# Kernel tuning notes

Hardware: AMD Instinct MI355X
Metric: run time of the kernel (lower is better)

## Reference

```python
import jax, jax.numpy as jnp
import numpy as np

N_DETS = 50000
K_NEIGH = 32
E = N_DETS * K_NEIGH  # 1,600,000 pairs


def _linear_params(key, fan_in, fan_out):
    kw, kb = jax.random.split(key)
    scale = 1.0 / np.sqrt(fan_in)
    W = jax.random.uniform(kw, (fan_in, fan_out), jnp.float32, -scale, scale)
    b = jax.random.uniform(kb, (fan_out,), jnp.float32, -scale, scale)
    return W, b


def setup_inputs() -> dict:
    key = jax.random.key(0)
    ks = jax.random.split(key, 10)
    detFeatures = jax.random.normal(ks[0], (N_DETS, 128), jnp.float32)
    # each detection is the center of exactly K_NEIGH pairs (sorted segment ids)
    cIdxs = jnp.repeat(jnp.arange(N_DETS, dtype=jnp.int32), K_NEIGH)
    nIdxs = jax.random.randint(ks[1], (E,), 0, N_DETS, jnp.int32)
    pairFeatures = jax.random.normal(ks[2], (E, 32), jnp.float32)
    W1, b1 = _linear_params(ks[3], 128, 32)   # fc1: 128 -> 32
    Wp0, bp0 = _linear_params(ks[4], 96, 64)  # pwfeat fc 0: 3*32 -> 64
    Wp1, bp1 = _linear_params(ks[5], 64, 64)  # pwfeat fc 1
    Wq0, bq0 = _linear_params(ks[6], 64, 64)  # postmax fc 0
    Wq1, bq1 = _linear_params(ks[7], 64, 64)  # postmax fc 1
    Wo, bo = _linear_params(ks[8], 64, 128)   # output FC: 64 -> 128
    return {"detFeatures": detFeatures, "cIdxs": cIdxs, "nIdxs": nIdxs,
            "pairFeatures": pairFeatures,
            "W1": W1, "b1": b1, "Wp0": Wp0, "bp0": bp0, "Wp1": Wp1, "bp1": bp1,
            "Wq0": Wq0, "bq0": bq0, "Wq1": Wq1, "bq1": bq1, "Wo": Wo, "bo": bo}


def reference(detFeatures, cIdxs, nIdxs, pairFeatures,
              W1, b1, Wp0, bp0, Wp1, bp1, Wq0, bq0, Wq1, bq1, Wo, bo):
    relu = jax.nn.relu
    # fc1 shortcut reduce: [N,128] -> [N,32]
    f1 = relu(detFeatures @ W1 + b1)
    # gather center/neighbor feats and concat with pair feats: [E, 96]
    comb = jnp.concatenate([pairFeatures, f1[cIdxs], f1[nIdxs]], axis=1)
    h = relu(comb @ Wp0 + bp0)   # [E, 64]
    h = relu(h @ Wp1 + bp1)      # [E, 64]
    # per-detection segment max (replaces the Python loop in the original)
    pooled = jax.ops.segment_max(h, cIdxs, num_segments=detFeatures.shape[0])
    p = relu(pooled @ Wq0 + bq0)
    p = relu(p @ Wq1 + bq1)
    refined = p @ Wo + bo        # [N, 128]
    return relu(detFeatures + refined)
```

## Files before the change

### kernel.cpp

```cpp
#include <hip/hip_runtime.h>
#include <hip/hip_bf16.h>

typedef __attribute__((ext_vector_type(4))) float f32x4;
typedef __attribute__((ext_vector_type(8))) short bf16x8;
typedef __attribute__((ext_vector_type(2))) unsigned int uint2v;

#define N_DETS  50000
#define E_PAIRS 1600000
#define NB64    (E_PAIRS / 64)

__device__ __forceinline__ unsigned short f2bf(float f){
  union { float f; unsigned int u; } v; v.f = f;
  return (unsigned short)((v.u + 0x7FFFu + ((v.u >> 16) & 1u)) >> 16);
}

__device__ __forceinline__ bf16x8 pack8(f32x4 a, f32x4 b){
  union { unsigned int u[4]; bf16x8 v; } t;
  t.u[0] = (unsigned int)f2bf(a[0]) | ((unsigned int)f2bf(a[1]) << 16);
  t.u[1] = (unsigned int)f2bf(a[2]) | ((unsigned int)f2bf(a[3]) << 16);
  t.u[2] = (unsigned int)f2bf(b[0]) | ((unsigned int)f2bf(b[1]) << 16);
  t.u[3] = (unsigned int)f2bf(b[2]) | ((unsigned int)f2bf(b[3]) << 16);
  return t.v;
}

__global__ __launch_bounds__(256) void kA(const float* __restrict__ det,
                                          const float* __restrict__ W1,
                                          const float* __restrict__ b1,
                                          unsigned short* __restrict__ f1){
  __shared__ float w[128*32];
  __shared__ float dt[16][132];
  const int t  = threadIdx.x;
  const int r0 = blockIdx.x * 16;
  {
    const f32x4* ws = reinterpret_cast<const f32x4*>(W1);
    #pragma unroll
    for (int i = 0; i < 4; ++i)
      reinterpret_cast<f32x4*>(w)[t + 256*i] = ws[t + 256*i];
    #pragma unroll
    for (int i = 0; i < 2; ++i){
      int idx = t + 256*i;
      int row = idx >> 5, c4 = (idx & 31) * 4;
      *reinterpret_cast<f32x4*>(&dt[row][c4]) =
        *reinterpret_cast<const f32x4*>(&det[(size_t)(r0+row)*128 + c4]);
    }
  }
  __syncthreads();
  const int r = t >> 4, c2 = (t & 15) * 2;
  float s0 = b1[c2], s1 = b1[c2 + 1];
  #pragma unroll 8
  for (int k = 0; k < 128; ++k){
    float d = dt[r][k];
    s0 = fmaf(d, w[k*32 + c2],     s0);
    s1 = fmaf(d, w[k*32 + c2 + 1], s1);
  }
  s0 = fmaxf(s0, 0.f); s1 = fmaxf(s1, 0.f);
  unsigned int pk = (unsigned int)f2bf(s0) | ((unsigned int)f2bf(s1) << 16);
  *reinterpret_cast<unsigned int*>(&f1[(size_t)(r0+r)*32 + c2]) = pk;
}

__global__ __launch_bounds__(256) void kPack(const float* __restrict__ Wp0,
                                             const float* __restrict__ Wp1,
                                             unsigned short* __restrict__ wf){
  int i = blockIdx.x * 256 + threadIdx.x;
  if (i >= 20*512) return;
  int f = i >> 9;
  int l = (i >> 3) & 63;
  int j = i & 7;
  int lc = l & 15, q = l >> 4;
  float v;
  if (f < 12){
    int kt = f >> 2, ot = f & 3;
    v = Wp0[(kt*32 + q*8 + j)*64 + ot*16 + lc];
  } else {
    int g = f - 12;
    int kt = g >> 2, n2 = g & 3;
    v = Wp1[(kt*32 + q*8 + j)*64 + n2*16 + lc];
  }
  wf[i] = f2bf(v);
}

__global__ __launch_bounds__(256) void kB(const float* __restrict__ pf,
                                          const int*   __restrict__ nIdxs,
                                          const unsigned short* __restrict__ f1,
                                          const unsigned short* __restrict__ wf,
                                          const float* __restrict__ bp0,
                                          const float* __restrict__ bp1,
                                          float* __restrict__ pooled){
  __shared__ __align__(16) unsigned short h1buf[4][4096];
  const int tid  = threadIdx.x;
  const int wid  = tid >> 6;
  const int lane = tid & 63;
  const int lc   = lane & 15;
  const int q    = lane >> 4;
  char* hb = reinterpret_cast<char*>(&h1buf[wid][0]);

  const bf16x8* wfv = reinterpret_cast<const bf16x8*>(wf);
  bf16x8 A0[3][4], B1w[2][4];
  #pragma unroll
  for (int kt = 0; kt < 3; ++kt)
    #pragma unroll
    for (int ot = 0; ot < 4; ++ot)
      A0[kt][ot] = wfv[(kt*4 + ot)*64 + lane];
  #pragma unroll
  for (int kt = 0; kt < 2; ++kt)
    #pragma unroll
    for (int n2 = 0; n2 < 4; ++n2)
      B1w[kt][n2] = wfv[(12 + kt*4 + n2)*64 + lane];

  f32x4 bb0[4];
  #pragma unroll
  for (int ot = 0; ot < 4; ++ot)
    bb0[ot] = *reinterpret_cast<const f32x4*>(&bp0[ot*16 + q*4]);
  float bb1[4];
  #pragma unroll
  for (int n2 = 0; n2 < 4; ++n2) bb1[n2] = bp1[n2*16 + lc];

  const int nwaves = gridDim.x * 4;
  for (int b = blockIdx.x*4 + wid; b < NB64; b += nwaves){
    const int e0 = b * 64;

    f32x4 acc[4][4];
    #pragma unroll
    for (int ot = 0; ot < 4; ++ot)
      #pragma unroll
      for (int et = 0; et < 4; ++et) acc[ot][et] = bb0[ot];

    #pragma unroll
    for (int et = 0; et < 4; ++et){
      const int eg = e0 + et*16 + lc;
      f32x4 p0 = *reinterpret_cast<const f32x4*>(&pf[(size_t)eg*32 + q*8]);
      f32x4 p1 = *reinterpret_cast<const f32x4*>(&pf[(size_t)eg*32 + q*8 + 4]);
      bf16x8 bfr0 = pack8(p0, p1);
      const int c = eg >> 5;
      bf16x8 bfr1 = *reinterpret_cast<const bf16x8*>(&f1[(size_t)c*32 + q*8]);
      const int n = nIdxs[eg];
      bf16x8 bfr2 = *reinterpret_cast<const bf16x8*>(&f1[(size_t)n*32 + q*8]);
      #pragma unroll
      for (int ot = 0; ot < 4; ++ot){
        acc[ot][et] = __builtin_amdgcn_mfma_f32_16x16x32_bf16(A0[0][ot], bfr0, acc[ot][et], 0,0,0);
        acc[ot][et] = __builtin_amdgcn_mfma_f32_16x16x32_bf16(A0[1][ot], bfr1, acc[ot][et], 0,0,0);
        acc[ot][et] = __builtin_amdgcn_mfma_f32_16x16x32_bf16(A0[2][ot], bfr2, acc[ot][et], 0,0,0);
      }
    }

    #pragma unroll
    for (int ot = 0; ot < 4; ++ot){
      #pragma unroll
      for (int et = 0; et < 4; ++et){
        f32x4 v = acc[ot][et];
        unsigned int lo = (unsigned int)f2bf(fmaxf(v[0],0.f)) | ((unsigned int)f2bf(fmaxf(v[1],0.f)) << 16);
        unsigned int hi = (unsigned int)f2bf(fmaxf(v[2],0.f)) | ((unsigned int)f2bf(fmaxf(v[3],0.f)) << 16);
        uint2v wv; wv[0] = lo; wv[1] = hi;
        int edge = et*16 + lc;
        int byte = (edge*128 + ot*32 + q*8) ^ ((edge & 7) << 4);
        *reinterpret_cast<uint2v*>(hb + byte) = wv;
      }
    }

    f32x4 acc2[4][4];
    #pragma unroll
    for (int m = 0; m < 4; ++m)
      #pragma unroll
      for (int n2 = 0; n2 < 4; ++n2){
        f32x4 ini = {bb1[n2], bb1[n2], bb1[n2], bb1[n2]};
        acc2[m][n2] = ini;
      }
    #pragma unroll
    for (int m = 0; m < 4; ++m){
      int edge = m*16 + lc;
      int swz  = (edge & 7) << 4;
      bf16x8 a0 = *reinterpret_cast<const bf16x8*>(hb + ((edge*128 + q*16)      ^ swz));
      bf16x8 a1 = *reinterpret_cast<const bf16x8*>(hb + ((edge*128 + 64 + q*16) ^ swz));
      #pragma unroll
      for (int n2 = 0; n2 < 4; ++n2){
        acc2[m][n2] = __builtin_amdgcn_mfma_f32_16x16x32_bf16(a0, B1w[0][n2], acc2[m][n2], 0,0,0);
        acc2[m][n2] = __builtin_amdgcn_mfma_f32_16x16x32_bf16(a1, B1w[1][n2], acc2[m][n2], 0,0,0);
      }
    }

    const int cbase = e0 >> 5;
    #pragma unroll
    for (int cen = 0; cen < 2; ++cen){
      float s0n, s1n, s2n, s3n;
      #pragma unroll
      for (int n2 = 0; n2 < 4; ++n2){
        float m0 = fmaxf(fmaxf(acc2[cen*2][n2][0], acc2[cen*2+1][n2][0]),
                         fmaxf(acc2[cen*2][n2][1], acc2[cen*2+1][n2][1]));
        float m1 = fmaxf(fmaxf(acc2[cen*2][n2][2], acc2[cen*2+1][n2][2]),
                         fmaxf(acc2[cen*2][n2][3], acc2[cen*2+1][n2][3]));
        float mm = fmaxf(m0, m1);
        mm = fmaxf(mm, __shfl_xor(mm, 16));
        mm = fmaxf(mm, __shfl_xor(mm, 32));
        if (n2 == 0) s0n = mm; else if (n2 == 1) s1n = mm; else if (n2 == 2) s2n = mm; else s3n = mm;
      }
      float v01 = (q & 1) ? s1n : s0n;
      float v23 = (q & 1) ? s3n : s2n;
      float v   = (q & 2) ? v23 : v01;
      v = fmaxf(v, 0.f);
      pooled[(size_t)(cbase + cen)*64 + lane] = v;
    }
  }
}

__global__ __launch_bounds__(256) void kC(const float* __restrict__ det,
                                          const float* __restrict__ pooled,
                                          const float* __restrict__ Wq0, const float* __restrict__ bq0,
                                          const float* __restrict__ Wq1, const float* __restrict__ bq1,
                                          const float* __restrict__ Wo,  const float* __restrict__ bo,
                                          float* __restrict__ out){
  __shared__ float w0[4096];
  __shared__ float w1[4096];
  __shared__ float wo2[8192];
  __shared__ float bb[256];
  __shared__ float pt[16*68];
  __shared__ float p1t[16*68];
  const int t  = threadIdx.x;
  const int r0 = blockIdx.x * 16;
  {
    const f32x4* s0 = reinterpret_cast<const f32x4*>(Wq0);
    const f32x4* s1 = reinterpret_cast<const f32x4*>(Wq1);
    const f32x4* s2 = reinterpret_cast<const f32x4*>(Wo);
    #pragma unroll
    for (int i = 0; i < 4; ++i) reinterpret_cast<f32x4*>(w0)[t + 256*i] = s0[t + 256*i];
    #pragma unroll
    for (int i = 0; i < 4; ++i) reinterpret_cast<f32x4*>(w1)[t + 256*i] = s1[t + 256*i];
    #pragma unroll
    for (int i = 0; i < 8; ++i) reinterpret_cast<f32x4*>(wo2)[t + 256*i] = s2[t + 256*i];
    if (t < 64)       bb[t] = bq0[t];
    else if (t < 128) bb[t] = bq1[t - 64];
    else              bb[t] = bo[t - 128];
    int row = t >> 4, c4l = (t & 15) * 4;
    *reinterpret_cast<f32x4*>(&pt[row*68 + c4l]) =
      *reinterpret_cast<const f32x4*>(&pooled[(size_t)(r0+row)*64 + c4l]);
  }
  __syncthreads();
  const int r  = t >> 4;
  const int c4 = (t & 15) * 4;

  f32x4 a = *reinterpret_cast<const f32x4*>(&bb[c4]);
  #pragma unroll 8
  for (int k = 0; k < 64; ++k){
    float pd = pt[r*68 + k];
    f32x4 wv = *reinterpret_cast<const f32x4*>(&w0[k*64 + c4]);
    a[0] = fmaf(pd, wv[0], a[0]); a[1] = fmaf(pd, wv[1], a[1]);
    a[2] = fmaf(pd, wv[2], a[2]); a[3] = fmaf(pd, wv[3], a[3]);
  }
  a[0]=fmaxf(a[0],0.f); a[1]=fmaxf(a[1],0.f); a[2]=fmaxf(a[2],0.f); a[3]=fmaxf(a[3],0.f);
  *reinterpret_cast<f32x4*>(&p1t[r*68 + c4]) = a;
  __syncthreads();

  f32x4 a2 = *reinterpret_cast<const f32x4*>(&bb[64 + c4]);
  #pragma unroll 8
  for (int k = 0; k < 64; ++k){
    float pd = p1t[r*68 + k];
    f32x4 wv = *reinterpret_cast<const f32x4*>(&w1[k*64 + c4]);
    a2[0] = fmaf(pd, wv[0], a2[0]); a2[1] = fmaf(pd, wv[1], a2[1]);
    a2[2] = fmaf(pd, wv[2], a2[2]); a2[3] = fmaf(pd, wv[3], a2[3]);
  }
  a2[0]=fmaxf(a2[0],0.f); a2[1]=fmaxf(a2[1],0.f); a2[2]=fmaxf(a2[2],0.f); a2[3]=fmaxf(a2[3],0.f);
  *reinterpret_cast<f32x4*>(&pt[r*68 + c4]) = a2;
  __syncthreads();

  f32x4 o0 = *reinterpret_cast<const f32x4*>(&bb[128 + c4]);
  f32x4 o1 = *reinterpret_cast<const f32x4*>(&bb[128 + 64 + c4]);
  #pragma unroll 8
  for (int k = 0; k < 64; ++k){
    float pd = pt[r*68 + k];
    f32x4 wa = *reinterpret_cast<const f32x4*>(&wo2[k*128 + c4]);
    f32x4 wb = *reinterpret_cast<const f32x4*>(&wo2[k*128 + 64 + c4]);
    o0[0] = fmaf(pd, wa[0], o0[0]); o0[1] = fmaf(pd, wa[1], o0[1]);
    o0[2] = fmaf(pd, wa[2], o0[2]); o0[3] = fmaf(pd, wa[3], o0[3]);
    o1[0] = fmaf(pd, wb[0], o1[0]); o1[1] = fmaf(pd, wb[1], o1[1]);
    o1[2] = fmaf(pd, wb[2], o1[2]); o1[3] = fmaf(pd, wb[3], o1[3]);
  }
  const float* dr = &det[(size_t)(r0 + r) * 128];
  f32x4 d0 = *reinterpret_cast<const f32x4*>(&dr[c4]);
  f32x4 d1 = *reinterpret_cast<const f32x4*>(&dr[64 + c4]);
  f32x4 res0, res1;
  res0[0]=fmaxf(d0[0]+o0[0],0.f); res0[1]=fmaxf(d0[1]+o0[1],0.f);
  res0[2]=fmaxf(d0[2]+o0[2],0.f); res0[3]=fmaxf(d0[3]+o0[3],0.f);
  res1[0]=fmaxf(d1[0]+o1[0],0.f); res1[1]=fmaxf(d1[1]+o1[1],0.f);
  res1[2]=fmaxf(d1[2]+o1[2],0.f); res1[3]=fmaxf(d1[3]+o1[3],0.f);
  float* orow = &out[(size_t)(r0 + r) * 128];
  *reinterpret_cast<f32x4*>(&orow[c4])      = res0;
  *reinterpret_cast<f32x4*>(&orow[64 + c4]) = res1;
}

extern "C" void kernel_launch(void* const* d_in, const int* in_sizes, int n_in,
                              void* d_out, int out_size, void* d_ws, size_t ws_size,
                              hipStream_t stream){
  const float* det   = (const float*)d_in[0];
  const int*   nIdx  = (const int*)  d_in[2];
  const float* pfeat = (const float*)d_in[3];
  const float* W1    = (const float*)d_in[4];
  const float* b1    = (const float*)d_in[5];
  const float* Wp0   = (const float*)d_in[6];
  const float* bp0   = (const float*)d_in[7];
  const float* Wp1   = (const float*)d_in[8];
  const float* bp1   = (const float*)d_in[9];
  const float* Wq0   = (const float*)d_in[10];
  const float* bq0   = (const float*)d_in[11];
  const float* Wq1   = (const float*)d_in[12];
  const float* bq1   = (const float*)d_in[13];
  const float* Wo    = (const float*)d_in[14];
  const float* bo    = (const float*)d_in[15];
  float* out = (float*)d_out;

  unsigned short* f1 = (unsigned short*)d_ws;
  unsigned short* wf = (unsigned short*)((char*)d_ws + 3200000);
  float* pooled      = (float*)((char*)d_ws + 3225600);

  kA   <<<N_DETS/16, 256, 0, stream>>>(det, W1, b1, f1);
  kPack<<<40,        256, 0, stream>>>(Wp0, Wp1, wf);
  kB   <<<1024,      256, 0, stream>>>(pfeat, nIdx, f1, wf, bp0, bp1, pooled);
  kC   <<<N_DETS/16, 256, 0, stream>>>(det, pooled, Wq0, bq0, Wq1, bq1, Wo, bo, out);
}
```

Baseline: 450.2 us.

## Fold weight packing into kA, restructure kB for occupancy, read kC weights directly

Moves the weight-packing kernel into the first blocks of kA, which removes one launch. kB is restructured: neighbor index loads are hoisted ahead of the first layer, accumulators are processed per edge tile, and the second layer is computed per center pair. The bp1 bias is now added after the max, which is valid because max commutes with adding a per-column constant. These changes cut register pressure so launch_bounds can request 3 blocks per SM, and the grid grows to 3125 blocks. kC no longer stages its weights in LDS and reads them through the cache, trading LDS traffic and occupancy limits for global and L1 reads.

```diff
diff --git a/kernel.cpp b/kernel.cpp
--- a/kernel.cpp
+++ b/kernel.cpp
@@ -26,7 +26,28 @@
 __global__ __launch_bounds__(256) void kA(const float* __restrict__ det,
                                           const float* __restrict__ W1,
                                           const float* __restrict__ b1,
-                                          unsigned short* __restrict__ f1){
+                                          const float* __restrict__ Wp0,
+                                          const float* __restrict__ Wp1,
+                                          unsigned short* __restrict__ f1,
+                                          unsigned short* __restrict__ wf){
+  if (blockIdx.x < 40){
+    int i = blockIdx.x * 256 + threadIdx.x;
+    int f = i >> 9;
+    int l = (i >> 3) & 63;
+    int j = i & 7;
+    int plc = l & 15, pq = l >> 4;
+    float v;
+    if (f < 12){
+      int kt = f >> 2, ot = f & 3;
+      v = Wp0[(kt*32 + pq*8 + j)*64 + ot*16 + plc];
+    } else {
+      int g = f - 12;
+      int kt = g >> 2, n2 = g & 3;
+      v = Wp1[(kt*32 + pq*8 + j)*64 + n2*16 + plc];
+    }
+    wf[i] = f2bf(v);
+  }
+
   __shared__ float w[128*32];
   __shared__ float dt[16][132];
   const int t  = threadIdx.x;
@@ -58,34 +79,13 @@
   *reinterpret_cast<unsigned int*>(&f1[(size_t)(r0+r)*32 + c2]) = pk;
 }
 
-__global__ __launch_bounds__(256) void kPack(const float* __restrict__ Wp0,
-                                             const float* __restrict__ Wp1,
-                                             unsigned short* __restrict__ wf){
-  int i = blockIdx.x * 256 + threadIdx.x;
-  if (i >= 20*512) return;
-  int f = i >> 9;
-  int l = (i >> 3) & 63;
-  int j = i & 7;
-  int lc = l & 15, q = l >> 4;
-  float v;
-  if (f < 12){
-    int kt = f >> 2, ot = f & 3;
-    v = Wp0[(kt*32 + q*8 + j)*64 + ot*16 + lc];
-  } else {
-    int g = f - 12;
-    int kt = g >> 2, n2 = g & 3;
-    v = Wp1[(kt*32 + q*8 + j)*64 + n2*16 + lc];
-  }
-  wf[i] = f2bf(v);
-}
-
-__global__ __launch_bounds__(256) void kB(const float* __restrict__ pf,
-                                          const int*   __restrict__ nIdxs,
-                                          const unsigned short* __restrict__ f1,
-                                          const unsigned short* __restrict__ wf,
-                                          const float* __restrict__ bp0,
-                                          const float* __restrict__ bp1,
-                                          float* __restrict__ pooled){
+__global__ __launch_bounds__(256, 3) void kB(const float* __restrict__ pf,
+                                             const int*   __restrict__ nIdxs,
+                                             const unsigned short* __restrict__ f1,
+                                             const unsigned short* __restrict__ wf,
+                                             const float* __restrict__ bp0,
+                                             const float* __restrict__ bp1,
+                                             float* __restrict__ pooled){
   __shared__ __align__(16) unsigned short h1buf[4][4096];
   const int tid  = threadIdx.x;
   const int wid  = tid >> 6;
@@ -111,83 +111,81 @@
   #pragma unroll
   for (int ot = 0; ot < 4; ++ot)
     bb0[ot] = *reinterpret_cast<const f32x4*>(&bp0[ot*16 + q*4]);
-  float bb1[4];
-  #pragma unroll
-  for (int n2 = 0; n2 < 4; ++n2) bb1[n2] = bp1[n2*16 + lc];
+  const float bb1s = bp1[lane];
 
   const int nwaves = gridDim.x * 4;
   for (int b = blockIdx.x*4 + wid; b < NB64; b += nwaves){
     const int e0 = b * 64;
 
-    f32x4 acc[4][4];
-    #pragma unroll
-    for (int ot = 0; ot < 4; ++ot)
-      #pragma unroll
-      for (int et = 0; et < 4; ++et) acc[ot][et] = bb0[ot];
+    int nid[4];
+    #pragma unroll
+    for (int et = 0; et < 4; ++et) nid[et] = nIdxs[e0 + et*16 + lc];
+    bf16x8 f1n[4];
+    #pragma unroll
+    for (int et = 0; et < 4; ++et)
+      f1n[et] = *reinterpret_cast<const bf16x8*>(&f1[(size_t)nid[et]*32 + q*8]);
 
     #pragma unroll
     for (int et = 0; et < 4; ++et){
       const int eg = e0 + et*16 + lc;
       f32x4 p0 = *reinterpret_cast<const f32x4*>(&pf[(size_t)eg*32 + q*8]);
       f32x4 p1 = *reinterpret_cast<const f32x4*>(&pf[(size_t)eg*32 + q*8 + 4]);
+      const int c = (e0 >> 5) + (et >> 1);
+      bf16x8 f1c = *reinterpret_cast<const bf16x8*>(&f1[(size_t)c*32 + q*8]);
       bf16x8 bfr0 = pack8(p0, p1);
-      const int c = eg >> 5;
-      bf16x8 bfr1 = *reinterpret_cast<const bf16x8*>(&f1[(size_t)c*32 + q*8]);
-      const int n = nIdxs[eg];
-      bf16x8 bfr2 = *reinterpret_cast<const bf16x8*>(&f1[(size_t)n*32 + q*8]);
+
+      f32x4 acc[4];
+      #pragma unroll
+      for (int ot = 0; ot < 4; ++ot) acc[ot] = bb0[ot];
       #pragma unroll
       for (int ot = 0; ot < 4; ++ot){
-        acc[ot][et] = __builtin_amdgcn_mfma_f32_16x16x32_bf16(A0[0][ot], bfr0, acc[ot][et], 0,0,0);
-        acc[ot][et] = __builtin_amdgcn_mfma_f32_16x16x32_bf16(A0[1][ot], bfr1, acc[ot][et], 0,0,0);
-        acc[ot][et] = __builtin_amdgcn_mfma_f32_16x16x32_bf16(A0[2][ot], bfr2, acc[ot][et], 0,0,0);
-      }
-    }
-
-    #pragma unroll
-    for (int ot = 0; ot < 4; ++ot){
-      #pragma unroll
-      for (int et = 0; et < 4; ++et){
-        f32x4 v = acc[ot][et];
+        acc[ot] = __builtin_amdgcn_mfma_f32_16x16x32_bf16(A0[0][ot], bfr0,    acc[ot], 0,0,0);
+        acc[ot] = __builtin_amdgcn_mfma_f32_16x16x32_bf16(A0[1][ot], f1c,     acc[ot], 0,0,0);
+        acc[ot] = __builtin_amdgcn_mfma_f32_16x16x32_bf16(A0[2][ot], f1n[et], acc[ot], 0,0,0);
+      }
+
+      const int edge = et*16 + lc;
+      const int swz  = (edge & 7) << 4;
+      #pragma unroll
+      for (int ot = 0; ot < 4; ++ot){
+        f32x4 v = acc[ot];
         unsigned int lo = (unsigned int)f2bf(fmaxf(v[0],0.f)) | ((unsigned int)f2bf(fmaxf(v[1],0.f)) << 16);
         unsigned int hi = (unsigned int)f2bf(fmaxf(v[2],0.f)) | ((unsigned int)f2bf(fmaxf(v[3],0.f)) << 16);
         uint2v wv; wv[0] = lo; wv[1] = hi;
-        int edge = et*16 + lc;
-        int byte = (edge*128 + ot*32 + q*8) ^ ((edge & 7) << 4);
-        *reinterpret_cast<uint2v*>(hb + byte) = wv;
-      }
-    }
-
-    f32x4 acc2[4][4];
-    #pragma unroll
-    for (int m = 0; m < 4; ++m)
+        *reinterpret_cast<uint2v*>(hb + ((edge*128 + ot*32 + q*8) ^ swz)) = wv;
+      }
+    }
+
+    const int cbase = e0 >> 5;
+    #pragma unroll
+    for (int cen = 0; cen < 2; ++cen){
+      const int eA = (2*cen)*16 + lc;
+      const int eB = (2*cen + 1)*16 + lc;
+      const int sw = (lc & 7) << 4;
+      bf16x8 a0A = *reinterpret_cast<const bf16x8*>(hb + ((eA*128      + q*16) ^ sw));
+      bf16x8 a1A = *reinterpret_cast<const bf16x8*>(hb + ((eA*128 + 64 + q*16) ^ sw));
+      bf16x8 a0B = *reinterpret_cast<const bf16x8*>(hb + ((eB*128      + q*16) ^ sw));
+      bf16x8 a1B = *reinterpret_cast<const bf16x8*>(hb + ((eB*128 + 64 + q*16) ^ sw));
+
+      f32x4 accA[4], accB[4];
       #pragma unroll
       for (int n2 = 0; n2 < 4; ++n2){
-        f32x4 ini = {bb1[n2], bb1[n2], bb1[n2], bb1[n2]};
-        acc2[m][n2] = ini;
-      }
-    #pragma unroll
-    for (int m = 0; m < 4; ++m){
-      int edge = m*16 + lc;
-      int swz  = (edge & 7) << 4;
-      bf16x8 a0 = *reinterpret_cast<const bf16x8*>(hb + ((edge*128 + q*16)      ^ swz));
-      bf16x8 a1 = *reinterpret_cast<const bf16x8*>(hb + ((edge*128 + 64 + q*16) ^ swz));
+        f32x4 z = {0.f, 0.f, 0.f, 0.f};
+        accA[n2] = z; accB[n2] = z;
+      }
       #pragma unroll
       for (int n2 = 0; n2 < 4; ++n2){
-        acc2[m][n2] = __builtin_amdgcn_mfma_f32_16x16x32_bf16(a0, B1w[0][n2], acc2[m][n2], 0,0,0);
-        acc2[m][n2] = __builtin_amdgcn_mfma_f32_16x16x32_bf16(a1, B1w[1][n2], acc2[m][n2], 0,0,0);
-      }
-    }
-
-    const int cbase = e0 >> 5;
-    #pragma unroll
-    for (int cen = 0; cen < 2; ++cen){
+        accA[n2] = __builtin_amdgcn_mfma_f32_16x16x32_bf16(a0A, B1w[0][n2], accA[n2], 0,0,0);
+        accA[n2] = __builtin_amdgcn_mfma_f32_16x16x32_bf16(a1A, B1w[1][n2], accA[n2], 0,0,0);
+        accB[n2] = __builtin_amdgcn_mfma_f32_16x16x32_bf16(a0B, B1w[0][n2], accB[n2], 0,0,0);
+        accB[n2] = __builtin_amdgcn_mfma_f32_16x16x32_bf16(a1B, B1w[1][n2], accB[n2], 0,0,0);
+      }
+
       float s0n, s1n, s2n, s3n;
       #pragma unroll
       for (int n2 = 0; n2 < 4; ++n2){
-        float m0 = fmaxf(fmaxf(acc2[cen*2][n2][0], acc2[cen*2+1][n2][0]),
-                         fmaxf(acc2[cen*2][n2][1], acc2[cen*2+1][n2][1]));
-        float m1 = fmaxf(fmaxf(acc2[cen*2][n2][2], acc2[cen*2+1][n2][2]),
-                         fmaxf(acc2[cen*2][n2][3], acc2[cen*2+1][n2][3]));
+        float m0 = fmaxf(fmaxf(accA[n2][0], accB[n2][0]), fmaxf(accA[n2][1], accB[n2][1]));
+        float m1 = fmaxf(fmaxf(accA[n2][2], accB[n2][2]), fmaxf(accA[n2][3], accB[n2][3]));
         float mm = fmaxf(m0, m1);
         mm = fmaxf(mm, __shfl_xor(mm, 16));
         mm = fmaxf(mm, __shfl_xor(mm, 32));
@@ -196,7 +194,7 @@
       float v01 = (q & 1) ? s1n : s0n;
       float v23 = (q & 1) ? s3n : s2n;
       float v   = (q & 2) ? v23 : v01;
-      v = fmaxf(v, 0.f);
+      v = fmaxf(v + bb1s, 0.f);
       pooled[(size_t)(cbase + cen)*64 + lane] = v;
     }
   }
@@ -208,27 +206,11 @@
                                           const float* __restrict__ Wq1, const float* __restrict__ bq1,
                                           const float* __restrict__ Wo,  const float* __restrict__ bo,
                                           float* __restrict__ out){
-  __shared__ float w0[4096];
-  __shared__ float w1[4096];
-  __shared__ float wo2[8192];
-  __shared__ float bb[256];
   __shared__ float pt[16*68];
   __shared__ float p1t[16*68];
   const int t  = threadIdx.x;
   const int r0 = blockIdx.x * 16;
   {
-    const f32x4* s0 = reinterpret_cast<const f32x4*>(Wq0);
-    const f32x4* s1 = reinterpret_cast<const f32x4*>(Wq1);
-    const f32x4* s2 = reinterpret_cast<const f32x4*>(Wo);
-    #pragma unroll
-    for (int i = 0; i < 4; ++i) reinterpret_cast<f32x4*>(w0)[t + 256*i] = s0[t + 256*i];
-    #pragma unroll
-    for (int i = 0; i < 4; ++i) reinterpret_cast<f32x4*>(w1)[t + 256*i] = s1[t + 256*i];
-    #pragma unroll
-    for (int i = 0; i < 8; ++i) reinterpret_cast<f32x4*>(wo2)[t + 256*i] = s2[t + 256*i];
-    if (t < 64)       bb[t] = bq0[t];
-    else if (t < 128) bb[t] = bq1[t - 64];
-    else              bb[t] = bo[t - 128];
     int row = t >> 4, c4l = (t & 15) * 4;
     *reinterpret_cast<f32x4*>(&pt[row*68 + c4l]) =
       *reinterpret_cast<const f32x4*>(&pooled[(size_t)(r0+row)*64 + c4l]);
@@ -237,11 +219,11 @@
   const int r  = t >> 4;
   const int c4 = (t & 15) * 4;
 
-  f32x4 a = *reinterpret_cast<const f32x4*>(&bb[c4]);
+  f32x4 a = *reinterpret_cast<const f32x4*>(&bq0[c4]);
   #pragma unroll 8
   for (int k = 0; k < 64; ++k){
     float pd = pt[r*68 + k];
-    f32x4 wv = *reinterpret_cast<const f32x4*>(&w0[k*64 + c4]);
+    f32x4 wv = *reinterpret_cast<const f32x4*>(&Wq0[k*64 + c4]);
     a[0] = fmaf(pd, wv[0], a[0]); a[1] = fmaf(pd, wv[1], a[1]);
     a[2] = fmaf(pd, wv[2], a[2]); a[3] = fmaf(pd, wv[3], a[3]);
   }
@@ -249,11 +231,11 @@
   *reinterpret_cast<f32x4*>(&p1t[r*68 + c4]) = a;
   __syncthreads();
 
-  f32x4 a2 = *reinterpret_cast<const f32x4*>(&bb[64 + c4]);
+  f32x4 a2 = *reinterpret_cast<const f32x4*>(&bq1[c4]);
   #pragma unroll 8
   for (int k = 0; k < 64; ++k){
     float pd = p1t[r*68 + k];
-    f32x4 wv = *reinterpret_cast<const f32x4*>(&w1[k*64 + c4]);
+    f32x4 wv = *reinterpret_cast<const f32x4*>(&Wq1[k*64 + c4]);
     a2[0] = fmaf(pd, wv[0], a2[0]); a2[1] = fmaf(pd, wv[1], a2[1]);
     a2[2] = fmaf(pd, wv[2], a2[2]); a2[3] = fmaf(pd, wv[3], a2[3]);
   }
@@ -261,13 +243,13 @@
   *reinterpret_cast<f32x4*>(&pt[r*68 + c4]) = a2;
   __syncthreads();
 
-  f32x4 o0 = *reinterpret_cast<const f32x4*>(&bb[128 + c4]);
-  f32x4 o1 = *reinterpret_cast<const f32x4*>(&bb[128 + 64 + c4]);
+  f32x4 o0 = *reinterpret_cast<const f32x4*>(&bo[c4]);
+  f32x4 o1 = *reinterpret_cast<const f32x4*>(&bo[64 + c4]);
   #pragma unroll 8
   for (int k = 0; k < 64; ++k){
     float pd = pt[r*68 + k];
-    f32x4 wa = *reinterpret_cast<const f32x4*>(&wo2[k*128 + c4]);
-    f32x4 wb = *reinterpret_cast<const f32x4*>(&wo2[k*128 + 64 + c4]);
+    f32x4 wa = *reinterpret_cast<const f32x4*>(&Wo[k*128 + c4]);
+    f32x4 wb = *reinterpret_cast<const f32x4*>(&Wo[k*128 + 64 + c4]);
     o0[0] = fmaf(pd, wa[0], o0[0]); o0[1] = fmaf(pd, wa[1], o0[1]);
     o0[2] = fmaf(pd, wa[2], o0[2]); o0[3] = fmaf(pd, wa[3], o0[3]);
     o1[0] = fmaf(pd, wb[0], o1[0]); o1[1] = fmaf(pd, wb[1], o1[1]);
@@ -310,8 +292,7 @@
   unsigned short* wf = (unsigned short*)((char*)d_ws + 3200000);
   float* pooled      = (float*)((char*)d_ws + 3225600);
 
-  kA   <<<N_DETS/16, 256, 0, stream>>>(det, W1, b1, f1);
-  kPack<<<40,        256, 0, stream>>>(Wp0, Wp1, wf);
-  kB   <<<1024,      256, 0, stream>>>(pfeat, nIdx, f1, wf, bp0, bp1, pooled);
-  kC   <<<N_DETS/16, 256, 0, stream>>>(det, pooled, Wq0, bq0, Wq1, bq1, Wo, bo, out);
-}
+  kA<<<N_DETS/16, 256, 0, stream>>>(det, W1, b1, Wp0, Wp1, f1, wf);
+  kB<<<3125,      256, 0, stream>>>(pfeat, nIdx, f1, wf, bp0, bp1, pooled);
+  kC<<<N_DETS/16, 256, 0, stream>>>(det, pooled, Wq0, bq0, Wq1, bq1, Wo, bo, out);
+}
```

After: 501.6 us. 11.4% more time.
